# Kernel tuning notes

Measured on AMD Instinct MI355X. Metric: run time of the kernel, lower is better.

## Reference

```python
import jax, jax.numpy as jnp
import numpy as np

B, N_IN, D, K, N = 8, 256, 128, 1024, 4096
EMA_GAMMA = 0.99


def setup_inputs() -> dict:
    key = jax.random.key(0)
    k1, k2, k3 = jax.random.split(key, 3)
    z = jax.random.normal(k1, (B, N_IN, N), dtype=jnp.float32)
    # Conv1d(n_in, d, 1, bias=False) == a (d, n_in) matmul; xavier-ish scale
    W_lin = jax.random.normal(k2, (D, N_IN), dtype=jnp.float32) * (1.0 / np.sqrt(N_IN))
    # codebook initialized xavier_uniform with gain=10 in the original
    lim = 10.0 * np.sqrt(6.0 / (K + D))
    emb = jax.random.uniform(k3, (K, D), dtype=jnp.float32, minval=-lim, maxval=lim)
    ema_numer = emb * (1.0 - EMA_GAMMA)
    ema_denom = jnp.ones((K,), dtype=jnp.float32) * (1.0 - EMA_GAMMA)
    return {"z": z, "W_lin": W_lin, "emb": emb,
            "ema_numer": ema_numer, "ema_denom": ema_denom}


def reference(z, W_lin, emb, ema_numer, ema_denom):
    # ze: (B, d, N) -- 1x1 conv == channel matmul
    ze = jnp.einsum('bcn,dc->bdn', z, W_lin)
    sg_emb = jax.lax.stop_gradient(emb)           # codebook is stop-gradded

    # scaled L2 distance:  ||ze - q|| / (||ze|| + ||q||), shape (B, K, N)
    ze_sq = jnp.sum(ze * ze, axis=1)              # (B, N)
    q_sq = jnp.sum(sg_emb * sg_emb, axis=1)       # (K,)
    dots = jnp.einsum('bdn,kd->bkn', ze, sg_emb)  # (B, K, N)
    dist_sq = jnp.maximum(ze_sq[:, None, :] + q_sq[None, :, None] - 2.0 * dots, 0.0)
    den = jnp.sqrt(ze_sq)[:, None, :] + jnp.sqrt(q_sq)[None, :, None]
    snorm = jnp.sqrt(dist_sq) / den               # (B, K, N)

    min_ind = jnp.argmin(snorm, axis=1)           # (B, N) int
    zq = jnp.moveaxis(sg_emb[min_ind], -1, 1)     # (B, d, N)

    # ReplaceGrad: forward value = zq, gradient routed to ze (straight-through)
    zq_rg = ze + jax.lax.stop_gradient(zq - ze)

    # EMA codebook statistics (scatter-add over codebook indices)
    flat_ind = min_ind.reshape(-1)                             # (B*N,)
    ze_flat = jax.lax.stop_gradient(
        jnp.moveaxis(ze, 1, 2).reshape(-1, ze.shape[1]))       # (B*N, d)
    z_sum = jax.ops.segment_sum(ze_flat, flat_ind, num_segments=K)   # (K, d)
    n_sum = jax.ops.segment_sum(jnp.ones(flat_ind.shape, ze.dtype),
                                flat_ind, num_segments=K)            # (K,)
    ema_numer_new = EMA_GAMMA * ema_numer + (1.0 - EMA_GAMMA) * z_sum
    ema_denom_new = EMA_GAMMA * ema_denom + (1.0 - EMA_GAMMA) * n_sum
    return zq_rg, ema_numer_new, ema_denom_new
```

## Files before the change

### kernel.cpp

```cpp
#include <hip/hip_runtime.h>
#include <cmath>
#include <stdint.h>

#define B_    8
#define NIN_  256
#define D_    128
#define K_    1024
#define N_    4096
#define P_    (B_ * N_)
#define MARGIN_M 1e-4f

typedef __attribute__((ext_vector_type(8))) short bf16x8;
typedef __attribute__((ext_vector_type(4))) float f32x4;

#define WS_ZSUM   0
#define WS_CNT    524288
#define WS_FLAGC  528384
#define WS_MEMSET 532480
#define WS_OFF    532480
#define WS_QSQ    536576
#define WS_QNORM  540672
#define WS_KSTAR  544768
#define WS_RANK   675840
#define WS_PLIST  806912
#define WS_KLIST  937984
#define WS_FLIST  1069056
#define WS_WT     1200128
#define WS_ZPM    1331200
#define WS_ZESQ   18108416
#define WS_ZEN    18239488
#define WS_ZE2F   18370560
#define WS_EMB2F  43536384
#define WS_VAL1   44322816
#define WS_IDX1   46419968
#define WS_VAL2   48517120

__device__ inline unsigned short f2bf(float v) {
  union { float f; uint32_t u; } c; c.f = v;
  return (unsigned short)((c.u + 0x7FFFu + ((c.u >> 16) & 1u)) >> 16);
}
__device__ inline float bf2f(unsigned short b) {
  union { float f; uint32_t u; } c; c.u = ((uint32_t)b) << 16; return c.f;
}
__device__ inline uint32_t pack2(float a, float b, int lo) {
  unsigned short ha = f2bf(a); if (lo) ha = f2bf(a - bf2f(ha));
  unsigned short hb = f2bf(b); if (lo) hb = f2bf(b - bf2f(hb));
  return (uint32_t)ha | ((uint32_t)hb << 16);
}

__global__ __launch_bounds__(256) void prep_kernel(
    const float* __restrict__ W, const float* __restrict__ emb,
    float* __restrict__ Wt, float* __restrict__ q_sq, float* __restrict__ q_norm,
    uint4* __restrict__ emb2f)
{
  const int tid = threadIdx.x;
  const int bid = blockIdx.x;
  if (bid < 128) {
    int t = bid * 256 + tid;
    int c = t >> 7, d = t & 127;
    Wt[t] = W[d * NIN_ + c];
  } else if (bid < 132) {
    int k = (bid - 128) * 256 + tid;
    const float* e = emb + (size_t)k * D_;
    float s = 0.f;
    #pragma unroll 8
    for (int d = 0; d < D_; ++d) s = fmaf(e[d], e[d], s);
    q_sq[k] = s;
    q_norm[k] = sqrtf(s);
  } else {
    const int kt = bid - 132;
    #pragma unroll
    for (int i = 0; i < 3; ++i) {
      int f    = i * 256 + tid;
      int c    = f >> 6;
      int lane = f & 63;
      int k    = kt * 16 + (lane & 15);
      int q    = lane >> 4;
      int kk0  = c * 32 + q * 8;
      int lo   = (kk0 >> 7) == 1;
      int d0   = kk0 & 127;
      float4 v0 = *(const float4*)&emb[(size_t)k * D_ + d0];
      float4 v1 = *(const float4*)&emb[(size_t)k * D_ + d0 + 4];
      uint4 u;
      u.x = pack2(v0.x, v0.y, lo);
      u.y = pack2(v0.z, v0.w, lo);
      u.z = pack2(v1.x, v1.y, lo);
      u.w = pack2(v1.z, v1.w, lo);
      emb2f[(size_t)kt * 768 + f] = u;
    }
  }
}

__global__ __launch_bounds__(512) void ze_kernel(
    const float* __restrict__ z, const float* __restrict__ Wt,
    float* __restrict__ ze_pm, float* __restrict__ ze_sq,
    float* __restrict__ ze_norm, uint4* __restrict__ ze2f)
{
  __shared__ float tile[64][132];
  __shared__ float sqpart[8][64];
  const int t    = threadIdx.x;
  const int lane = t & 63;
  const int wv   = __builtin_amdgcn_readfirstlane(t >> 6);
  const int p    = blockIdx.x * 64 + lane;
  const int b    = p >> 12;
  const int n    = p & (N_ - 1);

  float acc[16];
  #pragma unroll
  for (int j = 0; j < 16; ++j) acc[j] = 0.f;
  const float* zp = z + (size_t)b * NIN_ * N_ + n;
  const float* wp = Wt + wv * 16;
  #pragma unroll 4
  for (int c = 0; c < NIN_; ++c) {
    float zv = zp[(size_t)c * N_];
    #pragma unroll
    for (int j = 0; j < 16; ++j)
      acc[j] = fmaf(wp[c * D_ + j], zv, acc[j]);
  }
  #pragma unroll
  for (int j = 0; j < 16; ++j) tile[lane][wv * 16 + j] = acc[j];
  float s = 0.f;
  #pragma unroll
  for (int j = 0; j < 16; ++j) s = fmaf(acc[j], acc[j], s);
  sqpart[wv][lane] = s;
  __syncthreads();
  if (wv == 0) {
    float tt = sqpart[0][lane];
    #pragma unroll
    for (int w = 1; w < 8; ++w) tt += sqpart[w][lane];
    ze_sq[p] = tt;
    ze_norm[p] = sqrtf(tt);
  }
  const int row = t >> 5;
  const int c4  = (t & 31) * 4;
  #pragma unroll
  for (int r = 0; r < 4; ++r) {
    int pr = r * 16 + row;
    float4 v = *(const float4*)&tile[pr][c4];
    *(float4*)&ze_pm[(size_t)(blockIdx.x * 64 + pr) * D_ + c4] = v;
  }
  #pragma unroll
  for (int i = 0; i < 6; ++i) {
    int f    = i * 512 + t;
    int lane_f = f & 63;
    int g    = f >> 6;
    int c    = g % 12;
    int lpt  = g / 12;
    int pl   = lpt * 16 + (lane_f & 15);
    int q    = lane_f >> 4;
    int kk0  = c * 32 + q * 8;
    int lo   = (kk0 >> 7) == 2;
    int d0   = kk0 & 127;
    float4 v0 = *(const float4*)&tile[pl][d0];
    float4 v1 = *(const float4*)&tile[pl][d0 + 4];
    uint4 u;
    u.x = pack2(v0.x, v0.y, lo);
    u.y = pack2(v0.z, v0.w, lo);
    u.z = pack2(v1.x, v1.y, lo);
    u.w = pack2(v1.z, v1.w, lo);
    ze2f[((size_t)(blockIdx.x * 4 + lpt) * 12 + c) * 64 + lane_f] = u;
  }
}

__global__ __launch_bounds__(256, 3) void mfma_argmin_kernel(
    const uint4* __restrict__ ze2f, const uint4* __restrict__ emb2f,
    const float* __restrict__ ze_sq, const float* __restrict__ ze_norm,
    const float* __restrict__ q_sq, const float* __restrict__ q_norm,
    float* __restrict__ val1, int* __restrict__ idx1, float* __restrict__ val2)
{
  const int tid  = threadIdx.x;
  const int lane = tid & 63;
  const int w    = __builtin_amdgcn_readfirstlane(tid >> 6);
  const int x    = blockIdx.x & 7;
  const int ib   = blockIdx.x >> 3;
  const int pb2  = x * 64 + (ib & 63);
  const int kbb  = (ib >> 6) * 4 + w;

  const uint4* a_base = ze2f  + (size_t)pb2 * 3072 + lane;
  const uint4* b_base = emb2f + (size_t)kbb * 3072 + lane;

  f32x4 acc[4][4];
  #pragma unroll
  for (int ii = 0; ii < 4; ++ii)
    #pragma unroll
    for (int jj = 0; jj < 4; ++jj) acc[ii][jj] = (f32x4){0.f, 0.f, 0.f, 0.f};

  uint4 af[2][4], bf[2][4];
  #pragma unroll
  for (int ii = 0; ii < 4; ++ii) af[0][ii] = a_base[ii * 768];
  #pragma unroll
  for (int jj = 0; jj < 4; ++jj) bf[0][jj] = b_base[jj * 768];

  #pragma unroll
  for (int c = 0; c < 12; ++c) {
    const int cur = c & 1, nxt = cur ^ 1;
    if (c + 1 < 12) {
      #pragma unroll
      for (int ii = 0; ii < 4; ++ii)
        af[nxt][ii] = a_base[ii * 768 + (c + 1) * 64];
      #pragma unroll
      for (int jj = 0; jj < 4; ++jj)
        bf[nxt][jj] = b_base[jj * 768 + (c + 1) * 64];
    }
    #pragma unroll
    for (int ii = 0; ii < 4; ++ii) {
      union { uint4 u; bf16x8 h; } au; au.u = af[cur][ii];
      #pragma unroll
      for (int jj = 0; jj < 4; ++jj) {
        union { uint4 u; bf16x8 h; } bu; bu.u = bf[cur][jj];
        acc[ii][jj] = __builtin_amdgcn_mfma_f32_16x16x32_bf16(au.h, bu.h,
                                                              acc[ii][jj], 0, 0, 0);
      }
    }
  }

  const int col = lane & 15;
  const int q   = lane >> 4;
  float qsq_l[4], qn_l[4]; int kg[4];
  #pragma unroll
  for (int j = 0; j < 4; ++j) {
    kg[j]    = kbb * 64 + j * 16 + col;
    qsq_l[j] = q_sq[kg[j]];
    qn_l[j]  = q_norm[kg[j]];
  }
  const int g = kbb;
  #pragma unroll
  for (int ii = 0; ii < 4; ++ii) {
    const int pbase = pb2 * 64 + ii * 16 + q * 4;
    f32x4 zs = *(const f32x4*)&ze_sq[pbase];
    f32x4 zn = *(const f32x4*)&ze_norm[pbase];
    float m1r[4], m2r[4]; int k1r[4];
    #pragma unroll
    for (int r = 0; r < 4; ++r) { m1r[r] = 1e30f; m2r[r] = 1e30f; k1r[r] = 0; }
    #pragma unroll
    for (int j = 0; j < 4; ++j) {
      #pragma unroll
      for (int r = 0; r < 4; ++r) {
        float dsq = fmaxf(zs[r] + qsq_l[j] - 2.0f * acc[ii][j][r], 0.0f);
        float den = zn[r] + qn_l[j];
        float rd  = __builtin_amdgcn_rcpf(den);
        float m   = dsq * rd * rd;
        bool take = m < m1r[r];
        float loser = take ? m1r[r] : m;
        if (take) { m1r[r] = m; k1r[r] = kg[j]; }
        m2r[r] = fminf(m2r[r], loser);
      }
    }
    #pragma unroll
    for (int ms = 1; ms <= 8; ms <<= 1) {
      #pragma unroll
      for (int r = 0; r < 4; ++r) {
        float om1 = __shfl_xor(m1r[r], ms);
        int   ok1 = __shfl_xor(k1r[r], ms);
        float om2 = __shfl_xor(m2r[r], ms);
        bool take = (om1 < m1r[r]) || (om1 == m1r[r] && ok1 < k1r[r]);
        float loser = take ? m1r[r] : om1;
        if (take) { m1r[r] = om1; k1r[r] = ok1; }
        m2r[r] = fminf(fminf(m2r[r], om2), loser);
      }
    }
    if (col == 0) {
      const size_t o = (size_t)g * P_ + pbase;
      *(float4*)&val1[o] = make_float4(m1r[0], m1r[1], m1r[2], m1r[3]);
      *(int4*)&idx1[o]   = make_int4(k1r[0], k1r[1], k1r[2], k1r[3]);
      *(float4*)&val2[o] = make_float4(m2r[0], m2r[1], m2r[2], m2r[3]);
    }
  }
}

__global__ __launch_bounds__(256) void resolve_kernel(
    const float* __restrict__ val1, const int* __restrict__ idx1,
    const float* __restrict__ val2, int* __restrict__ kstar,
    int* __restrict__ rank, int* __restrict__ counts,
    int* __restrict__ flaglist, int* __restrict__ flagcnt)
{
  const int p = blockIdx.x * 256 + threadIdx.x;
  float m1 = 1e30f, m2 = 1e30f; int k1 = 0;
  #pragma unroll
  for (int g = 0; g < 16; ++g) {
    float v1 = val1[(size_t)g * P_ + p];
    int   i1 = idx1[(size_t)g * P_ + p];
    float v2 = val2[(size_t)g * P_ + p];
    bool take = v1 < m1;
    float loser = take ? m1 : v1;
    if (take) { m1 = v1; k1 = i1; }
    m2 = fminf(fminf(m2, v2), loser);
  }
  kstar[p] = k1;
  if (m2 - m1 <= MARGIN_M) {
    int s = atomicAdd(flagcnt, 1);
    flaglist[s] = p;
  } else {
    rank[p] = atomicAdd(&counts[k1], 1);
  }
}

__global__ __launch_bounds__(256) void fallback_kernel(
    const float* __restrict__ ze_pm, const float* __restrict__ emb,
    const float* __restrict__ ze_sq, const float* __restrict__ ze_norm,
    const float* __restrict__ q_sq, const float* __restrict__ q_norm,
    const int* __restrict__ flaglist, const int* __restrict__ flagcnt,
    int* __restrict__ kstar, int* __restrict__ rank, int* __restrict__ counts)
{
  __shared__ float zlds[128];
  __shared__ float wbs[4];
  __shared__ int   wbk[4];
  const int tid  = threadIdx.x;
  const int lane = tid & 63;
  const int w    = tid >> 6;
  const int cnt  = *flagcnt;
  for (int i = blockIdx.x; i < cnt; i += gridDim.x) {
    const int p = flaglist[i];
    __syncthreads();
    if (tid < 128) zlds[tid] = ze_pm[(size_t)p * D_ + tid];
    __syncthreads();
    const float zsq = ze_sq[p], zn = ze_norm[p];
    float bs = 1e30f; int bk = 0;
    #pragma unroll
    for (int tt = 0; tt < 4; ++tt) {
      const int k = (w * 4 + tt) * 64 + lane;
      const float* e = emb + (size_t)k * D_;
      float dot = 0.f;
      #pragma unroll 8
      for (int d = 0; d < D_; ++d)
        dot = fmaf(zlds[d], e[d], dot);
      float dsq = fmaxf(fmaf(-2.0f, dot, zsq + q_sq[k]), 0.0f);
      float sn  = sqrtf(dsq) / (zn + q_norm[k]);
      if (sn < bs) { bs = sn; bk = k; }
    }
    #pragma unroll
    for (int m = 1; m <= 32; m <<= 1) {
      float ov = __shfl_xor(bs, m);
      int   ok = __shfl_xor(bk, m);
      if (ov < bs || (ov == bs && ok < bk)) { bs = ov; bk = ok; }
    }
    if (lane == 0) { wbs[w] = bs; wbk[w] = bk; }
    __syncthreads();
    if (tid == 0) {
      float fb = wbs[0]; int fk = wbk[0];
      #pragma unroll
      for (int ww = 1; ww < 4; ++ww) {
        if (wbs[ww] < fb) { fb = wbs[ww]; fk = wbk[ww]; }
      }
      kstar[p] = fk;
      rank[p] = atomicAdd(&counts[fk], 1);
    }
  }
}

__global__ __launch_bounds__(1024) void prefix_kernel(
    const int* __restrict__ counts, const float* __restrict__ ema_denom,
    int* __restrict__ offsets, float* __restrict__ out_den)
{
  __shared__ int s[1024];
  const int t = threadIdx.x;
  const int c = counts[t];
  s[t] = c;
  __syncthreads();
  for (int off = 1; off < 1024; off <<= 1) {
    int v = (t >= off) ? s[t - off] : 0;
    __syncthreads();
    s[t] += v;
    __syncthreads();
  }
  offsets[t] = s[t] - c;
  out_den[t] = 0.99f * ema_denom[t] + 0.01f * (float)c;
}

__global__ __launch_bounds__(256) void scatter_kernel(
    const int* __restrict__ kstar, const int* __restrict__ rank,
    const int* __restrict__ offsets, int* __restrict__ pos_list,
    int* __restrict__ k_list)
{
  const int p = blockIdx.x * 256 + threadIdx.x;
  const int k = kstar[p];
  const int slot = offsets[k] + rank[p];
  pos_list[slot] = p;
  k_list[slot] = k;
}

__global__ __launch_bounds__(512) void zq_kernel(
    const float* __restrict__ ze_pm, const float* __restrict__ emb,
    const int* __restrict__ kstar, float* __restrict__ out)
{
  const int tid = threadIdx.x;
  const int lane = tid & 63;
  const int w = __builtin_amdgcn_readfirstlane(tid >> 6);
  const int p = blockIdx.x * 64 + lane;
  const int b = p >> 12;
  const int n = p & (N_ - 1);
  const int kst = kstar[p];
  const float* zr = ze_pm + (size_t)p * D_ + w * 16;
  const float* ek = emb + (size_t)kst * D_ + w * 16;
  float* op = out + (size_t)b * D_ * N_ + (size_t)(w * 16) * N_ + n;
  float4 zv[4], ev[4];
  #pragma unroll
  for (int r = 0; r < 4; ++r) {
    zv[r] = *(const float4*)&zr[r * 4];
    ev[r] = *(const float4*)&ek[r * 4];
  }
  #pragma unroll
  for (int r = 0; r < 4; ++r) {
    const float* zc = (const float*)&zv[r];
    const float* ec = (const float*)&ev[r];
    #pragma unroll
    for (int jj = 0; jj < 4; ++jj) {
      float zev = zc[jj];
      op[(size_t)(r * 4 + jj) * N_] = zev + (ec[jj] - zev);
    }
  }
}

__global__ __launch_bounds__(128) void gsum_kernel(
    const float* __restrict__ ze_pm, const int* __restrict__ pos_list,
    const int* __restrict__ k_list, float* __restrict__ z_sum)
{
  const int d  = threadIdx.x;
  const int i0 = blockIdx.x * 32;
  int   kprev = -1;
  float acc = 0.f;
  #pragma unroll
  for (int ii = 0; ii < 32; ++ii) {
    int p = pos_list[i0 + ii];
    int k = k_list[i0 + ii];
    if (k != kprev) {
      if (kprev >= 0) atomicAdd(&z_sum[(size_t)kprev * D_ + d], acc);
      acc = 0.f;
      kprev = k;
    }
    acc += ze_pm[(size_t)p * D_ + d];
  }
  if (kprev >= 0) atomicAdd(&z_sum[(size_t)kprev * D_ + d], acc);
}

__global__ __launch_bounds__(256) void finalize_num_kernel(
    const float* __restrict__ ema_numer, const float* __restrict__ z_sum,
    float* __restrict__ out)
{
  const int t = blockIdx.x * 256 + threadIdx.x;
  float* out_num = out + (size_t)B_ * D_ * N_;
  out_num[t] = 0.99f * ema_numer[t] + 0.01f * z_sum[t];
}

extern "C" void kernel_launch(void* const* d_in, const int* in_sizes, int n_in,
                              void* d_out, int out_size, void* d_ws, size_t ws_size,
                              hipStream_t stream)
{
  (void)in_sizes; (void)n_in; (void)out_size; (void)ws_size;
  const float* z         = (const float*)d_in[0];
  const float* W         = (const float*)d_in[1];
  const float* emb       = (const float*)d_in[2];
  const float* ema_numer = (const float*)d_in[3];
  const float* ema_denom = (const float*)d_in[4];
  float* out = (float*)d_out;
  char*  ws  = (char*)d_ws;
  float* z_sum   = (float*)(ws + WS_ZSUM);
  int*   counts  = (int*)(ws + WS_CNT);
  int*   flagcnt = (int*)(ws + WS_FLAGC);
  int*   offsets = (int*)(ws + WS_OFF);
  float* q_sq    = (float*)(ws + WS_QSQ);
  float* q_norm  = (float*)(ws + WS_QNORM);
  int*   kstar   = (int*)(ws + WS_KSTAR);
  int*   rank    = (int*)(ws + WS_RANK);
  int*   plist   = (int*)(ws + WS_PLIST);
  int*   klist   = (int*)(ws + WS_KLIST);
  int*   flist   = (int*)(ws + WS_FLIST);
  float* Wt      = (float*)(ws + WS_WT);
  float* ze_pm   = (float*)(ws + WS_ZPM);
  float* ze_sq   = (float*)(ws + WS_ZESQ);
  float* ze_norm = (float*)(ws + WS_ZEN);
  uint4* ze2f    = (uint4*)(ws + WS_ZE2F);
  uint4* emb2f   = (uint4*)(ws + WS_EMB2F);
  float* val1    = (float*)(ws + WS_VAL1);
  int*   idx1    = (int*)(ws + WS_IDX1);
  float* val2    = (float*)(ws + WS_VAL2);
  float* out_den = out + (size_t)B_ * D_ * N_ + K_ * D_;

  hipMemsetAsync(ws, 0, WS_MEMSET, stream);

  prep_kernel<<<196, 256, 0, stream>>>(W, emb, Wt, q_sq, q_norm, emb2f);
  ze_kernel<<<P_ / 64, 512, 0, stream>>>(z, Wt, ze_pm, ze_sq, ze_norm, ze2f);
  mfma_argmin_kernel<<<2048, 256, 0, stream>>>(ze2f, emb2f, ze_sq, ze_norm,
                                               q_sq, q_norm, val1, idx1, val2);
  resolve_kernel<<<P_ / 256, 256, 0, stream>>>(val1, idx1, val2, kstar,
                                               rank, counts, flist, flagcnt);
  fallback_kernel<<<1024, 256, 0, stream>>>(ze_pm, emb, ze_sq, ze_norm,
                                            q_sq, q_norm, flist, flagcnt,
                                            kstar, rank, counts);
  prefix_kernel<<<1, 1024, 0, stream>>>(counts, ema_denom, offsets, out_den);
  scatter_kernel<<<P_ / 256, 256, 0, stream>>>(kstar, rank, offsets, plist, klist);
  zq_kernel<<<P_ / 64, 512, 0, stream>>>(ze_pm, emb, kstar, out);
  gsum_kernel<<<P_ / 32, 128, 0, stream>>>(ze_pm, plist, klist, z_sum);
  finalize_num_kernel<<<K_ * D_ / 256, 256, 0, stream>>>(ema_numer, z_sum, out);
}
```

Measured before the change: 254.1 us.

## Stage MFMA operands through LDS with global_load_lds and fold memset into prep

The argmin GEMM kernel now loads A and B fragments cooperatively into double-buffered shared memory with direct global-to-LDS loads. Each block covers a 128x128 tile split into 2x2 waves, so each wave reuses shared operands instead of fetching its own 64x64 operands from global memory. The main loop uses barriers, waitcnt and priority hints, and occupancy is raised to 4 blocks. The separate hipMemsetAsync is replaced by extra prep_kernel blocks that zero the workspace, saving one launch. The cost is barrier overhead and LDS pressure per step.

```diff
diff --git a/kernel.cpp b/kernel.cpp
--- a/kernel.cpp
+++ b/kernel.cpp
@@ -48,10 +48,16 @@
   return (uint32_t)ha | ((uint32_t)hb << 16);
 }
 
+__device__ inline void gl_lds(const uint4* g, uint4* l) {
+  __builtin_amdgcn_global_load_lds(
+      (const __attribute__((address_space(1))) unsigned int*)g,
+      (__attribute__((address_space(3))) unsigned int*)l, 16, 0, 0);
+}
+
 __global__ __launch_bounds__(256) void prep_kernel(
     const float* __restrict__ W, const float* __restrict__ emb,
     float* __restrict__ Wt, float* __restrict__ q_sq, float* __restrict__ q_norm,
-    uint4* __restrict__ emb2f)
+    uint4* __restrict__ emb2f, uint4* __restrict__ wszero)
 {
   const int tid = threadIdx.x;
   const int bid = blockIdx.x;
@@ -67,7 +73,7 @@
     for (int d = 0; d < D_; ++d) s = fmaf(e[d], e[d], s);
     q_sq[k] = s;
     q_norm[k] = sqrtf(s);
-  } else {
+  } else if (bid < 196) {
     const int kt = bid - 132;
     #pragma unroll
     for (int i = 0; i < 3; ++i) {
@@ -88,6 +94,9 @@
       u.w = pack2(v1.z, v1.w, lo);
       emb2f[(size_t)kt * 768 + f] = u;
     }
+  } else {
+    int t = (bid - 196) * 256 + tid;
+    wszero[t] = make_uint4(0u, 0u, 0u, 0u);
   }
 }
 
@@ -162,22 +171,31 @@
   }
 }
 
-__global__ __launch_bounds__(256, 3) void mfma_argmin_kernel(
+__global__ __launch_bounds__(256, 4) void mfma_argmin_kernel(
     const uint4* __restrict__ ze2f, const uint4* __restrict__ emb2f,
     const float* __restrict__ ze_sq, const float* __restrict__ ze_norm,
     const float* __restrict__ q_sq, const float* __restrict__ q_norm,
     float* __restrict__ val1, int* __restrict__ idx1, float* __restrict__ val2)
 {
+  __shared__ uint4 Ls[2][16][64];
   const int tid  = threadIdx.x;
   const int lane = tid & 63;
   const int w    = __builtin_amdgcn_readfirstlane(tid >> 6);
   const int x    = blockIdx.x & 7;
   const int ib   = blockIdx.x >> 3;
-  const int pb2  = x * 64 + (ib & 63);
-  const int kbb  = (ib >> 6) * 4 + w;
-
-  const uint4* a_base = ze2f  + (size_t)pb2 * 3072 + lane;
-  const uint4* b_base = emb2f + (size_t)kbb * 3072 + lane;
+  const int pb3  = x * 32 + (ib & 31);
+  const int kb2  = ib >> 5;
+  const int pt0  = pb3 * 8;
+  const int ct0  = kb2 * 8;
+  const int wm   = w >> 1;
+  const int wn   = w & 1;
+  const int wq   = w * 4;
+  const int wm4  = wm * 4;
+  const int wn4  = wn * 4;
+
+  const uint4* sbase = (w < 2)
+      ? ze2f  + ((size_t)(pt0 + w * 4) * 12) * 64 + lane
+      : emb2f + ((size_t)(ct0 + (w - 2) * 4) * 12) * 64 + lane;
 
   f32x4 acc[4][4];
   #pragma unroll
@@ -185,48 +203,68 @@
     #pragma unroll
     for (int jj = 0; jj < 4; ++jj) acc[ii][jj] = (f32x4){0.f, 0.f, 0.f, 0.f};
 
-  uint4 af[2][4], bf[2][4];
-  #pragma unroll
-  for (int ii = 0; ii < 4; ++ii) af[0][ii] = a_base[ii * 768];
-  #pragma unroll
-  for (int jj = 0; jj < 4; ++jj) bf[0][jj] = b_base[jj * 768];
-
-  #pragma unroll
-  for (int c = 0; c < 12; ++c) {
-    const int cur = c & 1, nxt = cur ^ 1;
-    if (c + 1 < 12) {
-      #pragma unroll
-      for (int ii = 0; ii < 4; ++ii)
-        af[nxt][ii] = a_base[ii * 768 + (c + 1) * 64];
-      #pragma unroll
-      for (int jj = 0; jj < 4; ++jj)
-        bf[nxt][jj] = b_base[jj * 768 + (c + 1) * 64];
-    }
-    #pragma unroll
-    for (int ii = 0; ii < 4; ++ii) {
-      union { uint4 u; bf16x8 h; } au; au.u = af[cur][ii];
-      #pragma unroll
-      for (int jj = 0; jj < 4; ++jj) {
-        union { uint4 u; bf16x8 h; } bu; bu.u = bf[cur][jj];
-        acc[ii][jj] = __builtin_amdgcn_mfma_f32_16x16x32_bf16(au.h, bu.h,
-                                                              acc[ii][jj], 0, 0, 0);
-      }
-    }
-  }
+#define STAGE(NB, C)                                                        \
+  gl_lds(sbase + 0 * 768 + (C) * 64, &Ls[NB][wq + 0][0]);                   \
+  gl_lds(sbase + 1 * 768 + (C) * 64, &Ls[NB][wq + 1][0]);                   \
+  gl_lds(sbase + 2 * 768 + (C) * 64, &Ls[NB][wq + 2][0]);                   \
+  gl_lds(sbase + 3 * 768 + (C) * 64, &Ls[NB][wq + 3][0]);
+
+#define MFMA_STEP(CUR)                                                      \
+  {                                                                         \
+    uint4 afr[4], bfr[4];                                                   \
+    afr[0] = Ls[CUR][wm4 + 0][lane];  afr[1] = Ls[CUR][wm4 + 1][lane];      \
+    afr[2] = Ls[CUR][wm4 + 2][lane];  afr[3] = Ls[CUR][wm4 + 3][lane];      \
+    bfr[0] = Ls[CUR][8 + wn4 + 0][lane]; bfr[1] = Ls[CUR][8 + wn4 + 1][lane]; \
+    bfr[2] = Ls[CUR][8 + wn4 + 2][lane]; bfr[3] = Ls[CUR][8 + wn4 + 3][lane]; \
+    __builtin_amdgcn_s_setprio(1);                                          \
+    _Pragma("unroll")                                                       \
+    for (int ii = 0; ii < 4; ++ii) {                                        \
+      union { uint4 u; bf16x8 h; } au; au.u = afr[ii];                      \
+      _Pragma("unroll")                                                     \
+      for (int jj = 0; jj < 4; ++jj) {                                      \
+        union { uint4 u; bf16x8 h; } bu; bu.u = bfr[jj];                    \
+        acc[ii][jj] = __builtin_amdgcn_mfma_f32_16x16x32_bf16(au.h, bu.h,   \
+                                                        acc[ii][jj], 0, 0, 0); \
+      }                                                                     \
+    }                                                                       \
+    __builtin_amdgcn_s_setprio(0);                                          \
+  }
+
+#define STEP_MID(C, CUR, NXT)                                               \
+  STAGE(NXT, (C) + 1)                                                       \
+  asm volatile("s_waitcnt vmcnt(4)" ::: "memory");                          \
+  __builtin_amdgcn_s_barrier();                                             \
+  __builtin_amdgcn_sched_barrier(0);                                        \
+  MFMA_STEP(CUR)                                                            \
+  __builtin_amdgcn_s_barrier();                                             \
+  __builtin_amdgcn_sched_barrier(0);
+
+  STAGE(0, 0)
+  STEP_MID(0, 0, 1)  STEP_MID(1, 1, 0)  STEP_MID(2, 0, 1)  STEP_MID(3, 1, 0)
+  STEP_MID(4, 0, 1)  STEP_MID(5, 1, 0)  STEP_MID(6, 0, 1)  STEP_MID(7, 1, 0)
+  STEP_MID(8, 0, 1)  STEP_MID(9, 1, 0)  STEP_MID(10, 0, 1)
+  asm volatile("s_waitcnt vmcnt(0)" ::: "memory");
+  __builtin_amdgcn_s_barrier();
+  __builtin_amdgcn_sched_barrier(0);
+  MFMA_STEP(1)
+
+#undef STEP_MID
+#undef MFMA_STEP
+#undef STAGE
 
   const int col = lane & 15;
   const int q   = lane >> 4;
   float qsq_l[4], qn_l[4]; int kg[4];
   #pragma unroll
   for (int j = 0; j < 4; ++j) {
-    kg[j]    = kbb * 64 + j * 16 + col;
+    kg[j]    = kb2 * 128 + wn * 64 + j * 16 + col;
     qsq_l[j] = q_sq[kg[j]];
     qn_l[j]  = q_norm[kg[j]];
   }
-  const int g = kbb;
+  const int g = kb2 * 2 + wn;
   #pragma unroll
   for (int ii = 0; ii < 4; ++ii) {
-    const int pbase = pb2 * 64 + ii * 16 + q * 4;
+    const int pbase = pb3 * 128 + wm * 64 + ii * 16 + q * 4;
     f32x4 zs = *(const f32x4*)&ze_sq[pbase];
     f32x4 zn = *(const f32x4*)&ze_norm[pbase];
     float m1r[4], m2r[4]; int k1r[4];
@@ -476,9 +514,8 @@
   float* val2    = (float*)(ws + WS_VAL2);
   float* out_den = out + (size_t)B_ * D_ * N_ + K_ * D_;
 
-  hipMemsetAsync(ws, 0, WS_MEMSET, stream);
-
-  prep_kernel<<<196, 256, 0, stream>>>(W, emb, Wt, q_sq, q_norm, emb2f);
+  prep_kernel<<<326, 256, 0, stream>>>(W, emb, Wt, q_sq, q_norm, emb2f,
+                                       (uint4*)ws);
   ze_kernel<<<P_ / 64, 512, 0, stream>>>(z, Wt, ze_pm, ze_sq, ze_norm, ze2f);
   mfma_argmin_kernel<<<2048, 256, 0, stream>>>(ze2f, emb2f, ze_sq, ze_norm,
                                                q_sq, q_norm, val1, idx1, val2);
```

New measurement: 239.1 us. 5.9% less time.
